# Kernel tuning notes

Measured on AMD Instinct MI355X. Metric: run time of the kernel, lower is better.

The kernel has to match this reference:

```python
import jax, jax.numpy as jnp
from jax import lax
import numpy as np


def _conv4d(x, w, b, stride, padding):
    # Faithful 4D conv emulation: K temporal slices, each its own 3D conv.
    # x: [B,Ci,T,D,H,W]; w: [K,Co,Ci,k,k,k]; b: [K,Co] or None.
    # Quirk preserved: bias b[i] is added once per contributing temporal tap i
    # (the torch code accumulates full conv3d outputs including bias).
    B, Ci, T = x.shape[0], x.shape[1], x.shape[2]
    K = w.shape[0]
    O = (T + 2 * padding - K) // stride + 1
    out = None
    for i in range(K):
        j = np.arange(O) * stride + i - padding          # static input frame idx per output frame
        valid = (j >= 0) & (j < T)
        jc = np.clip(j, 0, T - 1)
        xg = jnp.moveaxis(x[:, :, jc], 2, 1)             # [B,O,Ci,D,H,W]
        xg = xg.reshape(B * O, Ci, x.shape[3], x.shape[4], x.shape[5])
        y = lax.conv_general_dilated(xg, w[i], (stride,) * 3, [(padding, padding)] * 3,
                                     dimension_numbers=('NCDHW', 'OIDHW', 'NCDHW'))
        if b is not None:
            y = y + b[i][None, :, None, None, None]
        y = y.reshape(B, O, y.shape[1], y.shape[2], y.shape[3], y.shape[4])
        y = y * jnp.asarray(valid, y.dtype)[None, :, None, None, None, None]
        out = y if out is None else out + y
    return jnp.moveaxis(out, 1, 2)                       # [B,Co,O,D',H',W']


def _maxpool4d(x, k, s, p):
    # pool3d-per-frame then pool1d over T == one 4D max pool (max commutes)
    return lax.reduce_window(x, jnp.array(-jnp.inf, x.dtype), lax.max,
                             (1, 1, k, k, k, k), (1, 1, s, s, s, s),
                             [(0, 0), (0, 0)] + [(p, p)] * 4)


def _avgpool4d_2(x):
    # avg-of-avgs over a full (2,2,2,2) window == 4D average
    s = lax.reduce_window(x, jnp.array(0.0, x.dtype), lax.add,
                          (1, 1, 2, 2, 2, 2), (1,) * 6, [(0, 0)] * 6)
    return s / jnp.asarray(16.0, x.dtype)


def _block(x, w1, b1, w2, b2, stride, dw):
    y = jax.nn.relu(_conv4d(x, w1, b1, stride, 1))
    y = _conv4d(y, w2, b2, 1, 1)
    res = x if dw is None else _conv4d(x, dw, None, stride, 0)
    return jax.nn.relu(y + res)


def _forward(x, conv1_w, l1_w1, l1_b1, l1_w2, l1_b2,
             l2_w1, l2_b1, l2_w2, l2_b2, l2_dw,
             l3_w1, l3_b1, l3_w2, l3_b2, l3_dw,
             l4_w1, l4_b1, l4_w2, l4_b2, l4_dw, fc_w, fc_b):
    h = x[:, None]                                       # [B,1,T,D,H,W]
    h = jax.nn.relu(_conv4d(h, conv1_w, None, 2, 3))     # 36 -> 18
    h = _maxpool4d(h, 3, 2, 1)                           # 18 -> 9
    h = _block(h, l1_w1, l1_b1, l1_w2, l1_b2, 1, None)   # 9
    h = _block(h, l2_w1, l2_b1, l2_w2, l2_b2, 2, l2_dw)  # 9 -> 5
    h = _block(h, l3_w1, l3_b1, l3_w2, l3_b2, 2, l3_dw)  # 5 -> 3
    h = _block(h, l4_w1, l4_b1, l4_w2, l4_b2, 2, l4_dw)  # 3 -> 2
    h = _avgpool4d_2(h)                                  # 2 -> 1
    h = h.reshape(-1, 512)
    return h @ fc_w.T + fc_b


def setup_inputs() -> dict:
    key = jax.random.key(0)
    ks = jax.random.split(key, 40)
    ctr = iter(range(40))
    def w(shape, fan):
        return jax.random.normal(ks[next(ctr)], shape, jnp.float32) * np.float32(np.sqrt(2.0 / fan))
    def bias(shape):
        return jax.random.normal(ks[next(ctr)], shape, jnp.float32) * np.float32(0.01)
    d = {}
    d['x'] = jax.random.normal(ks[next(ctr)], (1, 36, 36, 36, 36), jnp.float32)
    d['conv1_w'] = w((7, 64, 1, 7, 7, 7), 343)
    d['l1_w1'] = w((3, 64, 64, 3, 3, 3), 64 * 27); d['l1_b1'] = bias((3, 64))
    d['l1_w2'] = w((3, 64, 64, 3, 3, 3), 64 * 27); d['l1_b2'] = bias((3, 64))
    d['l2_w1'] = w((3, 128, 64, 3, 3, 3), 64 * 27); d['l2_b1'] = bias((3, 128))
    d['l2_w2'] = w((3, 128, 128, 3, 3, 3), 128 * 27); d['l2_b2'] = bias((3, 128))
    d['l2_dw'] = w((1, 128, 64, 1, 1, 1), 64)
    d['l3_w1'] = w((3, 256, 128, 3, 3, 3), 128 * 27); d['l3_b1'] = bias((3, 256))
    d['l3_w2'] = w((3, 256, 256, 3, 3, 3), 256 * 27); d['l3_b2'] = bias((3, 256))
    d['l3_dw'] = w((1, 256, 128, 1, 1, 1), 128)
    d['l4_w1'] = w((3, 512, 256, 3, 3, 3), 256 * 27); d['l4_b1'] = bias((3, 512))
    d['l4_w2'] = w((3, 512, 512, 3, 3, 3), 512 * 27); d['l4_b2'] = bias((3, 512))
    d['l4_dw'] = w((1, 512, 256, 1, 1, 1), 256)
    d['fc_w'] = w((1, 512), 512); d['fc_b'] = bias((1,))
    return d


def reference(x, conv1_w, l1_w1, l1_b1, l1_w2, l1_b2,
              l2_w1, l2_b1, l2_w2, l2_b2, l2_dw,
              l3_w1, l3_b1, l3_w2, l3_b2, l3_dw,
              l4_w1, l4_b1, l4_w2, l4_b2, l4_dw, fc_w, fc_b):
    return _forward(x, conv1_w, l1_w1, l1_b1, l1_w2, l1_b2,
                    l2_w1, l2_b1, l2_w2, l2_b2, l2_dw,
                    l3_w1, l3_b1, l3_w2, l3_b2, l3_dw,
                    l4_w1, l4_b1, l4_w2, l4_b2, l4_dw, fc_w, fc_b)
```

## Files before the change

### kernel.cpp

```cpp
#include <hip/hip_runtime.h>

typedef __bf16 bf16x8 __attribute__((ext_vector_type(8)));
typedef float f32x4 __attribute__((ext_vector_type(4)));
typedef unsigned short ushortT;

__device__ __forceinline__ unsigned short f2bf(float f) {
    unsigned u = __float_as_uint(f);
    u += 0x7fffu + ((u >> 16) & 1u);
    return (unsigned short)(u >> 16);
}
__device__ __forceinline__ float bf2f(unsigned short h) {
    return __uint_as_float((unsigned)h << 16);
}

__global__ __launch_bounds__(256) void prep0(const float* __restrict__ x,
                                             const float* __restrict__ c1w,
                                             ushortT* __restrict__ xp,
                                             ushortT* __restrict__ o1) {
    int bid = blockIdx.x, tid = threadIdx.x;
    if (bid < 1737) {
        long idx = (long)bid * 256 + tid;
        if (idx >= 444528L) return;
        int q = (int)(idx % 6); long r = idx / 6;
        int h = (int)(r % 42); r /= 42;
        int d = (int)(r % 42); int t = (int)(r / 42);
        int tt = t - 3, dd = d - 3, hh = h - 3;
        bool rok = ((unsigned)tt < 36u) && ((unsigned)dd < 36u) && ((unsigned)hh < 36u);
        const float* src = x + (((long)tt * 36 + dd) * 36 + hh) * 36;
        union { ushortT s[8]; uint4 u; } v;
#pragma unroll
        for (int j = 0; j < 8; ++j) {
            int ww = q * 8 + j - 3;
            float f = (rok && (unsigned)ww < 36u) ? src[ww] : 0.f;
            v.s[j] = f2bf(f);
        }
        *(uint4*)(xp + idx * 8) = v.u;
    } else {
        int e = (bid - 1737) * 256 + tid;
        if (e < 200704) {
            int k = e % 3136, co = e / 3136;
            int kw = k & 7, kh = (k >> 3) & 7, kdt = k >> 6;
            int kt = kdt / 7, kd = kdt % 7;
            float v = 0.f;
            if (kh < 7 && kw < 7)
                v = c1w[(size_t)(kt * 64 + co) * 343 + kd * 49 + kh * 7 + kw];
            o1[e] = f2bf(v);
        }
    }
}

__global__ __launch_bounds__(128) void mega_kernel(
        const ushortT* __restrict__ xp, const ushortT* __restrict__ aw,
        ushortT* __restrict__ outc1,
        const float* __restrict__ w11, const float* __restrict__ w12,
        const float* __restrict__ w21, const float* __restrict__ w22,
        const float* __restrict__ w31, const float* __restrict__ w32,
        const float* __restrict__ w41, const float* __restrict__ w42,
        ushortT* __restrict__ o11, ushortT* __restrict__ o12,
        ushortT* __restrict__ o21, ushortT* __restrict__ o22,
        ushortT* __restrict__ o31, ushortT* __restrict__ o32,
        ushortT* __restrict__ o41, ushortT* __restrict__ o42) {
    __shared__ __align__(16) ushortT smem[9520];
    int bid = blockIdx.x, tid = threadIdx.x;

    if (bid < 1350) {
        int wt = bid % 5; int r = bid / 5;
        int ht = r % 5; r /= 5;
        int dt = r % 3; int ot = r / 3;
        int ow0 = wt * 4, oh0 = ht * 4, od0 = dt * 6;
        int gw0 = 2 * ow0, gh0 = 2 * oh0, gd0 = 2 * od0;

        int lane = tid & 63, wv = tid >> 6;
        int l15 = lane & 15, g = lane >> 4;
        int dh = l15 >> 2, dw = l15 & 3;

        const ushortT* ap0 = aw + (size_t)(wv * 32 + l15) * 3136 + g * 8;
        const ushortT* ap1 = ap0 + 16 * 3136;

        ushortT* curb = smem;
        ushortT* nxtb = smem + 4760;

        auto stage = [&](ushortT* buf, int kt) {
            int gt = 2 * ot + kt;
            for (int rr = tid; rr < 238; rr += 128) {
                int ld = rr / 14, lh = rr - ld * 14;
                const ushortT* s = xp +
                    ((size_t)((gt * 42 + gd0 + ld) * 42 + gh0 + lh)) * 48 + gw0;
                uint4 a = *(const uint4*)s;
                uint4 b = *(const uint4*)(s + 8);
                ushortT* d = buf + rr * 20;
                *(uint2*)(d)      = make_uint2(a.x, a.y);
                *(uint2*)(d + 4)  = make_uint2(a.z, a.w);
                *(uint2*)(d + 8)  = make_uint2(b.x, b.y);
                *(uint2*)(d + 12) = make_uint2(b.z, b.w);
            }
        };

        f32x4 acc[2][6];
#pragma unroll
        for (int c = 0; c < 2; ++c)
#pragma unroll
            for (int m = 0; m < 6; ++m) acc[c][m] = (f32x4){0.f, 0.f, 0.f, 0.f};

        stage(curb, 0);
        __syncthreads();

        int lhl = (2 * dh + g) * 20 + 2 * dw;
        int kidx = 0;
        for (int kt = 0; kt < 7; ++kt) {
            if (kt < 6) stage(nxtb, kt + 1);
            for (int kd = 0; kd < 7; ++kd) {
                int C0 = kd * 280 + lhl;
#pragma unroll
                for (int khq = 0; khq < 2; ++khq) {
                    bf16x8 a0 = *(const bf16x8*)(ap0 + kidx);
                    bf16x8 a1 = *(const bf16x8*)(ap1 + kidx);
                    kidx += 32;
                    int C = C0 + khq * 80;
#pragma unroll
                    for (int m = 0; m < 6; ++m) {
                        int off = C + m * 560;
                        union { unsigned u[4]; bf16x8 v; } bb;
                        bb.u[0] = *(const unsigned*)(curb + off);
                        bb.u[1] = *(const unsigned*)(curb + off + 2);
                        bb.u[2] = *(const unsigned*)(curb + off + 4);
                        bb.u[3] = *(const unsigned*)(curb + off + 6);
                        acc[0][m] = __builtin_amdgcn_mfma_f32_16x16x32_bf16(a0, bb.v, acc[0][m], 0, 0, 0);
                        acc[1][m] = __builtin_amdgcn_mfma_f32_16x16x32_bf16(a1, bb.v, acc[1][m], 0, 0, 0);
                    }
                }
            }
            __syncthreads();
            ushortT* t2 = curb; curb = nxtb; nxtb = t2;
        }

        int oh = oh0 + dh, ow = ow0 + dw;
        if (oh < 18 && ow < 18) {
#pragma unroll
            for (int m = 0; m < 6; ++m) {
                int od = od0 + m;
                int pos = ((ot * 18 + od) * 18 + oh) * 18 + ow;
#pragma unroll
                for (int c = 0; c < 2; ++c) {
                    ushort4 st;
                    st.x = f2bf(fmaxf(acc[c][m][0], 0.f));
                    st.y = f2bf(fmaxf(acc[c][m][1], 0.f));
                    st.z = f2bf(fmaxf(acc[c][m][2], 0.f));
                    st.w = f2bf(fmaxf(acc[c][m][3], 0.f));
                    *(ushort4*)(outc1 + (size_t)pos * 64 + wv * 32 + c * 16 + g * 4) = st;
                }
            }
        }
        return;
    }

    int wb = bid - 1350;
    const float* in; ushortT* out; int Ci, Co, nc, base;
    if (wb < 1536) {
        if (wb < 384) {
            if (wb < 192) { in = w11; out = o11; Ci = 64; Co = 64; nc = 1; base = 0; }
            else          { in = w12; out = o12; Ci = 64; Co = 64; nc = 1; base = 192; }
        } else if (wb < 768) { in = w21; out = o21; Ci = 64;  Co = 128; nc = 1; base = 384; }
        else                 { in = w22; out = o22; Ci = 128; Co = 128; nc = 2; base = 768; }
    } else if (wb < 6144) {
        if (wb < 3072) { in = w31; out = o31; Ci = 128; Co = 256; nc = 2; base = 1536; }
        else           { in = w32; out = o32; Ci = 256; Co = 256; nc = 4; base = 3072; }
    } else {
        if (wb < 12288) { in = w41; out = o41; Ci = 256; Co = 512; nc = 4; base = 6144; }
        else            { in = w42; out = o42; Ci = 512; Co = 512; nc = 8; base = 12288; }
    }
    int lb = wb - base;
    int c64 = lb % nc;
    int co = (lb / nc) % Co;
    int i = lb / (nc * Co);

    const float* src = in + ((size_t)(i * Co + co) * Ci + 64 * c64) * 27;
    float* tile = (float*)smem;
    for (int e = tid; e < 432; e += 128)
        *(float4*)(tile + 4 * e) = *(const float4*)(src + 4 * e);
    __syncthreads();
    ushortT* dst = out + (size_t)(i * 27) * Co * Ci + (size_t)co * Ci + 64 * c64;
    size_t tapstride = (size_t)Co * Ci;
    for (int e = tid; e < 432; e += 128) {
        int tap = e >> 4, q = e & 15;
        ushort4 v;
        v.x = f2bf(tile[(4 * q + 0) * 27 + tap]);
        v.y = f2bf(tile[(4 * q + 1) * 27 + tap]);
        v.z = f2bf(tile[(4 * q + 2) * 27 + tap]);
        v.w = f2bf(tile[(4 * q + 3) * 27 + tap]);
        *(ushort4*)(dst + (size_t)tap * tapstride + 4 * q) = v;
    }
}

__global__ void maxpool2(const ushortT* __restrict__ in, ushortT* __restrict__ out,
                         ushortT* __restrict__ zb) {
    int idx = blockIdx.x * 256 + threadIdx.x;
    if (idx < 128) zb[idx] = 0;
    if (idx >= 6561 * 16) return;
    int c4 = idx & 15;
    int p = idx >> 4;
    int ow = p % 9; int t = p / 9;
    int oh = t % 9; t /= 9;
    int od = t % 9; int ot = t / 9;
    ushort4 m = {0, 0, 0, 0};
    for (int kt = 0; kt < 3; ++kt) { int it = 2 * ot + kt - 1; if ((unsigned)it >= 18u) continue;
        for (int kd = 0; kd < 3; ++kd) { int id = 2 * od + kd - 1; if ((unsigned)id >= 18u) continue;
            for (int kh = 0; kh < 3; ++kh) { int ih = 2 * oh + kh - 1; if ((unsigned)ih >= 18u) continue;
                int rb = ((it * 18 + id) * 18 + ih) * 18;
                for (int kw = 0; kw < 3; ++kw) { int iw = 2 * ow + kw - 1; if ((unsigned)iw >= 18u) continue;
                    ushort4 v = *(const ushort4*)(in + (size_t)(rb + iw) * 64 + c4 * 4);
                    m.x = v.x > m.x ? v.x : m.x;
                    m.y = v.y > m.y ? v.y : m.y;
                    m.z = v.z > m.z ? v.z : m.z;
                    m.w = v.w > m.w ? v.w : m.w;
                }
            }
        }
    }
    *(ushort4*)(out + (size_t)p * 64 + c4 * 4) = m;
}

template <int KC, int FUSE>
__global__ void convmfma(const ushortT* __restrict__ xb, const ushortT* __restrict__ wt,
                         const float* __restrict__ bias, const ushortT* __restrict__ res,
                         ushortT* __restrict__ outb, float* __restrict__ part,
                         const ushortT* __restrict__ zq,
                         int Ci, int Co, int T, int O, int stride, int chunk,
                         const float* __restrict__ dwW, ushortT* __restrict__ dwOut) {
    if (dwW && blockIdx.y == (unsigned)(Co >> 6)) {
        int O2 = O * O, O3 = O2 * O, O4 = O3 * O;
        int total = Co * O4;
        int sthr = gridDim.x * gridDim.z * 256;
        for (int idx = (blockIdx.z * gridDim.x + blockIdx.x) * 256 + threadIdx.x;
             idx < total; idx += sthr) {
            int co = idx % Co;
            int pos = idx / Co;
            int ow = pos % O, oh = (pos / O) % O, od = (pos / O2) % O, ot = pos / O3;
            int ip = (((2 * ot) * T + 2 * od) * T + 2 * oh) * T + 2 * ow;
            const ushortT* xpp = xb + (size_t)ip * Ci;
            const float* wp = dwW + (size_t)co * Ci;
            float acc = 0.f;
            for (int c8 = 0; c8 < Ci; c8 += 8) {
                uint4 xv = *(const uint4*)(xpp + c8);
                float4 w0 = *(const float4*)(wp + c8);
                float4 w1 = *(const float4*)(wp + c8 + 4);
                acc = fmaf(bf2f((unsigned short)(xv.x & 0xffff)), w0.x, acc);
                acc = fmaf(bf2f((unsigned short)(xv.x >> 16)),    w0.y, acc);
                acc = fmaf(bf2f((unsigned short)(xv.y & 0xffff)), w0.z, acc);
                acc = fmaf(bf2f((unsigned short)(xv.y >> 16)),    w0.w, acc);
                acc = fmaf(bf2f((unsigned short)(xv.z & 0xffff)), w1.x, acc);
                acc = fmaf(bf2f((unsigned short)(xv.z >> 16)),    w1.y, acc);
                acc = fmaf(bf2f((unsigned short)(xv.w & 0xffff)), w1.z, acc);
                acc = fmaf(bf2f((unsigned short)(xv.w >> 16)),    w1.w, acc);
            }
            dwOut[idx] = f2bf(acc);
        }
        return;
    }

    int lane = threadIdx.x & 63;
    int wv = threadIdx.x >> 6;
    int p0 = blockIdx.x * 16;
    int co0 = (blockIdx.y * 4 + wv) * 16;
    int cbase = blockIdx.z * chunk;

    int pn = p0 + (lane & 15);
    int O2 = O * O, O3 = O2 * O, O4 = O3 * O;
    bool pv = pn < O4;
    int pc = pv ? pn : 0;
    int ow = pc % O, oh = (pc / O) % O, od = (pc / O2) % O, ot = pc / O3;
    int g = lane >> 4;
    int kl = cbase + g * 8;

    const ushortT* aRow = wt + (size_t)(co0 + (lane & 15)) * Ci + kl;
    size_t tapStride = (size_t)Co * Ci;
    const ushortT* zp = zq + g * 8;

    f32x4 acc = {0.f, 0.f, 0.f, 0.f};

    int itb = ot * stride - 1, idb = od * stride - 1, ihb = oh * stride - 1, iwb = ow * stride - 1;

    for (int i = 0; i < 3; ++i) {
        int it = itb + i;
        bool vt = pv && ((unsigned)it < (unsigned)T);
        for (int kd = 0; kd < 3; ++kd) {
            int id = idb + kd;
            bool vdd = vt && ((unsigned)id < (unsigned)T);
            int btd = (it * T + id) * T;
            for (int kh = 0; kh < 3; ++kh) {
                int ih = ihb + kh;
                bool vh = vdd && ((unsigned)ih < (unsigned)T);
                for (int kw = 0; kw < 3; ++kw) {
                    int iw = iwb + kw;
                    bool v = vh && ((unsigned)iw < (unsigned)T);
                    int ip = (btd + ih) * T + iw;
                    const ushortT* bp = v ? (xb + (size_t)ip * Ci + kl) : zp;
                    int tapIdx = (i * 9 + kd * 3 + kh) * 3 + kw;
                    const ushortT* apw = aRow + (size_t)tapIdx * tapStride;
#pragma unroll
                    for (int kc = 0; kc < KC; ++kc) {
                        bf16x8 av = *(const bf16x8*)(apw + kc * 32);
                        bf16x8 bv = *(const bf16x8*)(bp + kc * 32);
                        acc = __builtin_amdgcn_mfma_f32_16x16x32_bf16(av, bv, acc, 0, 0, 0);
                    }
                }
            }
        }
    }

    if (!pv) return;
    int cob = co0 + g * 4;
    if (FUSE) {
        float bb[4] = {0.f, 0.f, 0.f, 0.f};
        for (int i = 0; i < 3; ++i) {
            int it = itb + i;
            if ((unsigned)it < (unsigned)T) {
#pragma unroll
                for (int r = 0; r < 4; ++r) bb[r] += bias[i * Co + cob + r];
            }
        }
        float rv[4] = {0.f, 0.f, 0.f, 0.f};
        if (res) {
            ushort4 rr = *(const ushort4*)(res + (size_t)pn * Co + cob);
            rv[0] = bf2f(rr.x); rv[1] = bf2f(rr.y); rv[2] = bf2f(rr.z); rv[3] = bf2f(rr.w);
        }
        ushort4 st;
        st.x = f2bf(fmaxf(acc[0] + bb[0] + rv[0], 0.f));
        st.y = f2bf(fmaxf(acc[1] + bb[1] + rv[1], 0.f));
        st.z = f2bf(fmaxf(acc[2] + bb[2] + rv[2], 0.f));
        st.w = f2bf(fmaxf(acc[3] + bb[3] + rv[3], 0.f));
        *(ushort4*)(outb + (size_t)pn * Co + cob) = st;
    } else {
        *(f32x4*)(part + ((size_t)blockIdx.z * O4 + pn) * Co + cob) = acc;
    }
}

__global__ void finalize_k(const float* __restrict__ part, int KS,
                           const float* __restrict__ bias, const ushortT* __restrict__ res,
                           ushortT* __restrict__ outb, int Co, int O4, int T, int O, int stride,
                           int total) {
    int idx = blockIdx.x * 256 + threadIdx.x;
    if (idx >= total) return;
    int co = idx % Co;
    int pos = idx / Co;
    float v = 0.f;
    for (int z = 0; z < KS; ++z) v += part[((size_t)z * O4 + pos) * Co + co];
    int ot = pos / (O * O * O);
    for (int i = 0; i < 3; ++i) {
        int it = ot * stride + i - 1;
        if ((unsigned)it < (unsigned)T) v += bias[i * Co + co];
    }
    if (res) v += bf2f(res[idx]);
    outb[idx] = f2bf(fmaxf(v, 0.f));
}

__global__ void avgfc2(const ushortT* __restrict__ xin, const float* __restrict__ fw,
                       const float* __restrict__ fb, float* __restrict__ out) {
    __shared__ float ls[8];
    int t = threadIdx.x;
    float s = 0.f;
#pragma unroll
    for (int pp = 0; pp < 16; ++pp) s += bf2f(xin[pp * 512 + t]);
    s = s * (1.f / 16.f) * fw[t];
    for (int off = 32; off > 0; off >>= 1) s += __shfl_xor(s, off, 64);
    if ((t & 63) == 0) ls[t >> 6] = s;
    __syncthreads();
    if (t == 0) {
        float tot = 0.f;
#pragma unroll
        for (int i = 0; i < 8; ++i) tot += ls[i];
        out[0] = tot + fb[0];
    }
}

extern "C" void kernel_launch(void* const* d_in, const int* in_sizes, int n_in,
                              void* d_out, int out_size, void* d_ws, size_t ws_size,
                              hipStream_t stream) {
    const float* x       = (const float*)d_in[0];
    const float* conv1_w = (const float*)d_in[1];
    const float* l1_w1 = (const float*)d_in[2];
    const float* l1_b1 = (const float*)d_in[3];
    const float* l1_w2 = (const float*)d_in[4];
    const float* l1_b2 = (const float*)d_in[5];
    const float* l2_w1 = (const float*)d_in[6];
    const float* l2_b1 = (const float*)d_in[7];
    const float* l2_w2 = (const float*)d_in[8];
    const float* l2_b2 = (const float*)d_in[9];
    const float* l2_dw = (const float*)d_in[10];
    const float* l3_w1 = (const float*)d_in[11];
    const float* l3_b1 = (const float*)d_in[12];
    const float* l3_w2 = (const float*)d_in[13];
    const float* l3_b2 = (const float*)d_in[14];
    const float* l3_dw = (const float*)d_in[15];
    const float* l4_w1 = (const float*)d_in[16];
    const float* l4_b1 = (const float*)d_in[17];
    const float* l4_w2 = (const float*)d_in[18];
    const float* l4_b2 = (const float*)d_in[19];
    const float* l4_dw = (const float*)d_in[20];
    const float* fc_w  = (const float*)d_in[21];
    const float* fc_b  = (const float*)d_in[22];
    float* outp = (float*)d_out;

    char* bp = (char*)d_ws;
    auto alloc = [&](size_t bytes) {
        char* r = bp;
        bp += (bytes + 255) & ~(size_t)255;
        return (void*)r;
    };
    ushortT* A16 = (ushortT*)alloc(6718464ull * 2);
    ushortT* XP  = (ushortT*)alloc(3556224ull * 2);
    ushortT* Aw1 = (ushortT*)alloc(200704ull * 2);
    ushortT* X0 = (ushortT*)alloc(419904ull * 2);
    ushortT* Y1 = (ushortT*)alloc(419904ull * 2);
    ushortT* X1 = (ushortT*)alloc(419904ull * 2);
    ushortT* Y2 = (ushortT*)alloc(80000ull * 2);
    ushortT* R2 = (ushortT*)alloc(80000ull * 2);
    ushortT* X2 = (ushortT*)alloc(80000ull * 2);
    ushortT* Y3 = (ushortT*)alloc(20736ull * 2);
    ushortT* R3 = (ushortT*)alloc(20736ull * 2);
    ushortT* X3 = (ushortT*)alloc(20736ull * 2);
    ushortT* Y4 = (ushortT*)alloc(8192ull * 2);
    ushortT* R4 = (ushortT*)alloc(8192ull * 2);
    ushortT* X4 = (ushortT*)alloc(8192ull * 2);
    ushortT* W11 = (ushortT*)alloc(331776ull * 2);
    ushortT* W12 = (ushortT*)alloc(331776ull * 2);
    ushortT* W21 = (ushortT*)alloc(663552ull * 2);
    ushortT* W22 = (ushortT*)alloc(1327104ull * 2);
    ushortT* W31 = (ushortT*)alloc(2654208ull * 2);
    ushortT* W32 = (ushortT*)alloc(5308416ull * 2);
    ushortT* W41 = (ushortT*)alloc(10616832ull * 2);
    ushortT* W42 = (ushortT*)alloc(21233664ull * 2);
    float* P    = (float*)alloc(165888ull * 4);
    ushortT* ZB = (ushortT*)alloc(256);
    if ((size_t)(bp - (char*)d_ws) > ws_size) return;

    prep0<<<2521, 256, 0, stream>>>(x, conv1_w, XP, Aw1);

    mega_kernel<<<25926, 128, 0, stream>>>(XP, Aw1, A16,
                                           l1_w1, l1_w2, l2_w1, l2_w2, l3_w1, l3_w2,
                                           l4_w1, l4_w2,
                                           W11, W12, W21, W22, W31, W32, W41, W42);

    maxpool2<<<411, 256, 0, stream>>>(A16, X0, ZB);

    convmfma<2, 1><<<dim3(411, 1, 1), 256, 0, stream>>>(X0, W11, l1_b1, nullptr, Y1, nullptr,
                                                        ZB, 64, 64, 9, 9, 1, 64,
                                                        nullptr, nullptr);
    convmfma<2, 1><<<dim3(411, 1, 1), 256, 0, stream>>>(Y1, W12, l1_b2, X0, X1, nullptr,
                                                        ZB, 64, 64, 9, 9, 1, 64,
                                                        nullptr, nullptr);

    convmfma<2, 1><<<dim3(40, 3, 1), 256, 0, stream>>>(X1, W21, l2_b1, nullptr, Y2, nullptr,
                                                       ZB, 64, 128, 9, 5, 2, 64,
                                                       l2_dw, R2);
    convmfma<4, 1><<<dim3(40, 2, 1), 256, 0, stream>>>(Y2, W22, l2_b2, R2, X2, nullptr,
                                                       ZB, 128, 128, 5, 5, 1, 128,
                                                       nullptr, nullptr);

    convmfma<1, 0><<<dim3(6, 5, 4), 256, 0, stream>>>(X2, W31, nullptr, nullptr, nullptr, P,
                                                      ZB, 128, 256, 5, 3, 2, 32,
                                                      l3_dw, R3);
    finalize_k<<<81, 256, 0, stream>>>(P, 4, l3_b1, nullptr, Y3, 256, 81, 5, 3, 2, 20736);
    convmfma<1, 0><<<dim3(6, 4, 8), 256, 0, stream>>>(Y3, W32, nullptr, nullptr, nullptr, P,
                                                      ZB, 256, 256, 3, 3, 1, 32,
                                                      nullptr, nullptr);
    finalize_k<<<81, 256, 0, stream>>>(P, 8, l3_b2, R3, X3, 256, 81, 3, 3, 1, 20736);

    convmfma<1, 0><<<dim3(1, 9, 8), 256, 0, stream>>>(X3, W41, nullptr, nullptr, nullptr, P,
                                                      ZB, 256, 512, 3, 2, 2, 32,
                                                      l4_dw, R4);
    finalize_k<<<32, 256, 0, stream>>>(P, 8, l4_b1, nullptr, Y4, 512, 16, 3, 2, 2, 8192);
    convmfma<1, 0><<<dim3(1, 8, 16), 256, 0, stream>>>(Y4, W42, nullptr, nullptr, nullptr, P,
                                                       ZB, 512, 512, 2, 2, 1, 32,
                                                       nullptr, nullptr);
    finalize_k<<<32, 256, 0, stream>>>(P, 16, l4_b2, R4, X4, 512, 16, 2, 2, 1, 8192);

    avgfc2<<<1, 512, 0, stream>>>(X4, fc_w, fc_b, outp);
}
```

Baseline: 547.2 us.

## Fuse trunk layers into one persistent kernel with grid barriers; pad conv1 smem rows

Replaces the chain of maxpool, per-layer convmfma, finalize and avgfc launches with a single persistent kernel of 512 blocks. Stages are separated by a software grid barrier built on atomics, which removes per-launch overhead and gaps between the many small late layers. Also pads the conv1 shared-memory row stride from 20 to 22 elements to reduce LDS bank conflicts. The cost is that convolution units lose their compile-time KC unrolling, and the grid barrier relies on all 512 blocks being co-resident, otherwise it can deadlock.

New measurement: 1.164 ms. 113% more time.

```diff
diff --git a/kernel.cpp b/kernel.cpp
--- a/kernel.cpp
+++ b/kernel.cpp
@@ -3,6 +3,8 @@
 typedef __bf16 bf16x8 __attribute__((ext_vector_type(8)));
 typedef float f32x4 __attribute__((ext_vector_type(4)));
 typedef unsigned short ushortT;
+
+#define NB 512
 
 __device__ __forceinline__ unsigned short f2bf(float f) {
     unsigned u = __float_as_uint(f);
@@ -16,8 +18,14 @@
 __global__ __launch_bounds__(256) void prep0(const float* __restrict__ x,
                                              const float* __restrict__ c1w,
                                              ushortT* __restrict__ xp,
-                                             ushortT* __restrict__ o1) {
+                                             ushortT* __restrict__ o1,
+                                             ushortT* __restrict__ zb,
+                                             int* __restrict__ bar) {
     int bid = blockIdx.x, tid = threadIdx.x;
+    if (bid == 0) {
+        if (tid < 128) zb[tid] = 0;
+        if (tid == 128) { bar[0] = 0; bar[1] = 0; }
+    }
     if (bid < 1737) {
         long idx = (long)bid * 256 + tid;
         if (idx >= 444528L) return;
@@ -60,7 +68,7 @@
         ushortT* __restrict__ o21, ushortT* __restrict__ o22,
         ushortT* __restrict__ o31, ushortT* __restrict__ o32,
         ushortT* __restrict__ o41, ushortT* __restrict__ o42) {
-    __shared__ __align__(16) ushortT smem[9520];
+    __shared__ __align__(16) ushortT smem[10472];
     int bid = blockIdx.x, tid = threadIdx.x;
 
     if (bid < 1350) {
@@ -78,7 +86,7 @@
         const ushortT* ap1 = ap0 + 16 * 3136;
 
         ushortT* curb = smem;
-        ushortT* nxtb = smem + 4760;
+        ushortT* nxtb = smem + 5236;
 
         auto stage = [&](ushortT* buf, int kt) {
             int gt = 2 * ot + kt;
@@ -88,11 +96,9 @@
                     ((size_t)((gt * 42 + gd0 + ld) * 42 + gh0 + lh)) * 48 + gw0;
                 uint4 a = *(const uint4*)s;
                 uint4 b = *(const uint4*)(s + 8);
-                ushortT* d = buf + rr * 20;
-                *(uint2*)(d)      = make_uint2(a.x, a.y);
-                *(uint2*)(d + 4)  = make_uint2(a.z, a.w);
-                *(uint2*)(d + 8)  = make_uint2(b.x, b.y);
-                *(uint2*)(d + 12) = make_uint2(b.z, b.w);
+                unsigned* d = (unsigned*)buf + rr * 11;
+                d[0] = a.x; d[1] = a.y; d[2] = a.z; d[3] = a.w;
+                d[4] = b.x; d[5] = b.y; d[6] = b.z; d[7] = b.w;
             }
         };
 
@@ -105,21 +111,21 @@
         stage(curb, 0);
         __syncthreads();
 
-        int lhl = (2 * dh + g) * 20 + 2 * dw;
+        int lhl = (2 * dh + g) * 22 + 2 * dw;
         int kidx = 0;
         for (int kt = 0; kt < 7; ++kt) {
             if (kt < 6) stage(nxtb, kt + 1);
             for (int kd = 0; kd < 7; ++kd) {
-                int C0 = kd * 280 + lhl;
+                int C0 = kd * 308 + lhl;
 #pragma unroll
                 for (int khq = 0; khq < 2; ++khq) {
                     bf16x8 a0 = *(const bf16x8*)(ap0 + kidx);
                     bf16x8 a1 = *(const bf16x8*)(ap1 + kidx);
                     kidx += 32;
-                    int C = C0 + khq * 80;
+                    int C = C0 + khq * 88;
 #pragma unroll
                     for (int m = 0; m < 6; ++m) {
-                        int off = C + m * 560;
+                        int off = C + m * 616;
                         union { unsigned u[4]; bf16x8 v; } bb;
                         bb.u[0] = *(const unsigned*)(curb + off);
                         bb.u[1] = *(const unsigned*)(curb + off + 2);
@@ -192,77 +198,35 @@
     }
 }
 
-__global__ void maxpool2(const ushortT* __restrict__ in, ushortT* __restrict__ out,
-                         ushortT* __restrict__ zb) {
-    int idx = blockIdx.x * 256 + threadIdx.x;
-    if (idx < 128) zb[idx] = 0;
-    if (idx >= 6561 * 16) return;
-    int c4 = idx & 15;
-    int p = idx >> 4;
-    int ow = p % 9; int t = p / 9;
-    int oh = t % 9; t /= 9;
-    int od = t % 9; int ot = t / 9;
-    ushort4 m = {0, 0, 0, 0};
-    for (int kt = 0; kt < 3; ++kt) { int it = 2 * ot + kt - 1; if ((unsigned)it >= 18u) continue;
-        for (int kd = 0; kd < 3; ++kd) { int id = 2 * od + kd - 1; if ((unsigned)id >= 18u) continue;
-            for (int kh = 0; kh < 3; ++kh) { int ih = 2 * oh + kh - 1; if ((unsigned)ih >= 18u) continue;
-                int rb = ((it * 18 + id) * 18 + ih) * 18;
-                for (int kw = 0; kw < 3; ++kw) { int iw = 2 * ow + kw - 1; if ((unsigned)iw >= 18u) continue;
-                    ushort4 v = *(const ushort4*)(in + (size_t)(rb + iw) * 64 + c4 * 4);
-                    m.x = v.x > m.x ? v.x : m.x;
-                    m.y = v.y > m.y ? v.y : m.y;
-                    m.z = v.z > m.z ? v.z : m.z;
-                    m.w = v.w > m.w ? v.w : m.w;
-                }
-            }
-        }
-    }
-    *(ushort4*)(out + (size_t)p * 64 + c4 * 4) = m;
-}
-
-template <int KC, int FUSE>
-__global__ void convmfma(const ushortT* __restrict__ xb, const ushortT* __restrict__ wt,
-                         const float* __restrict__ bias, const ushortT* __restrict__ res,
-                         ushortT* __restrict__ outb, float* __restrict__ part,
-                         const ushortT* __restrict__ zq,
-                         int Ci, int Co, int T, int O, int stride, int chunk,
-                         const float* __restrict__ dwW, ushortT* __restrict__ dwOut) {
-    if (dwW && blockIdx.y == (unsigned)(Co >> 6)) {
-        int O2 = O * O, O3 = O2 * O, O4 = O3 * O;
-        int total = Co * O4;
-        int sthr = gridDim.x * gridDim.z * 256;
-        for (int idx = (blockIdx.z * gridDim.x + blockIdx.x) * 256 + threadIdx.x;
-             idx < total; idx += sthr) {
-            int co = idx % Co;
-            int pos = idx / Co;
-            int ow = pos % O, oh = (pos / O) % O, od = (pos / O2) % O, ot = pos / O3;
-            int ip = (((2 * ot) * T + 2 * od) * T + 2 * oh) * T + 2 * ow;
-            const ushortT* xpp = xb + (size_t)ip * Ci;
-            const float* wp = dwW + (size_t)co * Ci;
-            float acc = 0.f;
-            for (int c8 = 0; c8 < Ci; c8 += 8) {
-                uint4 xv = *(const uint4*)(xpp + c8);
-                float4 w0 = *(const float4*)(wp + c8);
-                float4 w1 = *(const float4*)(wp + c8 + 4);
-                acc = fmaf(bf2f((unsigned short)(xv.x & 0xffff)), w0.x, acc);
-                acc = fmaf(bf2f((unsigned short)(xv.x >> 16)),    w0.y, acc);
-                acc = fmaf(bf2f((unsigned short)(xv.y & 0xffff)), w0.z, acc);
-                acc = fmaf(bf2f((unsigned short)(xv.y >> 16)),    w0.w, acc);
-                acc = fmaf(bf2f((unsigned short)(xv.z & 0xffff)), w1.x, acc);
-                acc = fmaf(bf2f((unsigned short)(xv.z >> 16)),    w1.y, acc);
-                acc = fmaf(bf2f((unsigned short)(xv.w & 0xffff)), w1.z, acc);
-                acc = fmaf(bf2f((unsigned short)(xv.w >> 16)),    w1.w, acc);
-            }
-            dwOut[idx] = f2bf(acc);
-        }
-        return;
-    }
-
+
+__device__ __forceinline__ void gbar(int* cnt, int* gen) {
+    __syncthreads();
+    if (threadIdx.x == 0) {
+        __threadfence();
+        int g = atomicAdd(gen, 0);
+        if (atomicAdd(cnt, 1) == NB - 1) {
+            atomicExch(cnt, 0);
+            __threadfence();
+            atomicAdd(gen, 1);
+        } else {
+            while (atomicAdd(gen, 0) == g) __builtin_amdgcn_s_sleep(2);
+        }
+        __threadfence();
+    }
+    __syncthreads();
+}
+
+__device__ __noinline__ void conv_unit(const ushortT* xb, const ushortT* wt,
+                                       const float* bias, const ushortT* res,
+                                       ushortT* outb, float* part, const ushortT* zq,
+                                       int Ci, int Co, int T, int O, int stride, int chunk,
+                                       int pblk, int cog, int ks, bool fuse) {
     int lane = threadIdx.x & 63;
     int wv = threadIdx.x >> 6;
-    int p0 = blockIdx.x * 16;
-    int co0 = (blockIdx.y * 4 + wv) * 16;
-    int cbase = blockIdx.z * chunk;
+    int p0 = pblk * 16;
+    int co0 = (cog * 4 + wv) * 16;
+    int cbase = ks * chunk;
+    int nkc = chunk >> 5;
 
     int pn = p0 + (lane & 15);
     int O2 = O * O, O3 = O2 * O, O4 = O3 * O;
@@ -297,8 +261,7 @@
                     const ushortT* bp = v ? (xb + (size_t)ip * Ci + kl) : zp;
                     int tapIdx = (i * 9 + kd * 3 + kh) * 3 + kw;
                     const ushortT* apw = aRow + (size_t)tapIdx * tapStride;
-#pragma unroll
-                    for (int kc = 0; kc < KC; ++kc) {
+                    for (int kc = 0; kc < nkc; ++kc) {
                         bf16x8 av = *(const bf16x8*)(apw + kc * 32);
                         bf16x8 bv = *(const bf16x8*)(bp + kc * 32);
                         acc = __builtin_amdgcn_mfma_f32_16x16x32_bf16(av, bv, acc, 0, 0, 0);
@@ -310,19 +273,19 @@
 
     if (!pv) return;
     int cob = co0 + g * 4;
-    if (FUSE) {
+    if (fuse) {
         float bb[4] = {0.f, 0.f, 0.f, 0.f};
         for (int i = 0; i < 3; ++i) {
             int it = itb + i;
             if ((unsigned)it < (unsigned)T) {
 #pragma unroll
-                for (int r = 0; r < 4; ++r) bb[r] += bias[i * Co + cob + r];
+                for (int rr = 0; rr < 4; ++rr) bb[rr] += bias[i * Co + cob + rr];
             }
         }
         float rv[4] = {0.f, 0.f, 0.f, 0.f};
         if (res) {
-            ushort4 rr = *(const ushort4*)(res + (size_t)pn * Co + cob);
-            rv[0] = bf2f(rr.x); rv[1] = bf2f(rr.y); rv[2] = bf2f(rr.z); rv[3] = bf2f(rr.w);
+            ushort4 r4 = *(const ushort4*)(res + (size_t)pn * Co + cob);
+            rv[0] = bf2f(r4.x); rv[1] = bf2f(r4.y); rv[2] = bf2f(r4.z); rv[3] = bf2f(r4.w);
         }
         ushort4 st;
         st.x = f2bf(fmaxf(acc[0] + bb[0] + rv[0], 0.f));
@@ -331,45 +294,169 @@
         st.w = f2bf(fmaxf(acc[3] + bb[3] + rv[3], 0.f));
         *(ushort4*)(outb + (size_t)pn * Co + cob) = st;
     } else {
-        *(f32x4*)(part + ((size_t)blockIdx.z * O4 + pn) * Co + cob) = acc;
-    }
-}
-
-__global__ void finalize_k(const float* __restrict__ part, int KS,
-                           const float* __restrict__ bias, const ushortT* __restrict__ res,
-                           ushortT* __restrict__ outb, int Co, int O4, int T, int O, int stride,
-                           int total) {
-    int idx = blockIdx.x * 256 + threadIdx.x;
-    if (idx >= total) return;
-    int co = idx % Co;
-    int pos = idx / Co;
-    float v = 0.f;
-    for (int z = 0; z < KS; ++z) v += part[((size_t)z * O4 + pos) * Co + co];
-    int ot = pos / (O * O * O);
-    for (int i = 0; i < 3; ++i) {
-        int it = ot * stride + i - 1;
-        if ((unsigned)it < (unsigned)T) v += bias[i * Co + co];
-    }
-    if (res) v += bf2f(res[idx]);
-    outb[idx] = f2bf(fmaxf(v, 0.f));
-}
-
-__global__ void avgfc2(const ushortT* __restrict__ xin, const float* __restrict__ fw,
-                       const float* __restrict__ fb, float* __restrict__ out) {
-    __shared__ float ls[8];
-    int t = threadIdx.x;
-    float s = 0.f;
-#pragma unroll
-    for (int pp = 0; pp < 16; ++pp) s += bf2f(xin[pp * 512 + t]);
-    s = s * (1.f / 16.f) * fw[t];
-    for (int off = 32; off > 0; off >>= 1) s += __shfl_xor(s, off, 64);
-    if ((t & 63) == 0) ls[t >> 6] = s;
-    __syncthreads();
-    if (t == 0) {
-        float tot = 0.f;
-#pragma unroll
-        for (int i = 0; i < 8; ++i) tot += ls[i];
-        out[0] = tot + fb[0];
+        *(f32x4*)(part + ((size_t)ks * O4 + pn) * Co + cob) = acc;
+    }
+}
+
+__device__ __noinline__ void dw_all(const ushortT* xb, const float* w, ushortT* out,
+                                    int Ci, int Co, int T, int O, int total) {
+    int O2 = O * O, O3 = O2 * O;
+    for (int idx = blockIdx.x * 256 + threadIdx.x; idx < total; idx += NB * 256) {
+        int co = idx % Co;
+        int pos = idx / Co;
+        int ow = pos % O, oh = (pos / O) % O, od = (pos / O2) % O, ot = pos / O3;
+        int ip = (((2 * ot) * T + 2 * od) * T + 2 * oh) * T + 2 * ow;
+        const ushortT* xp = xb + (size_t)ip * Ci;
+        const float* wp = w + (size_t)co * Ci;
+        float acc = 0.f;
+        for (int c8 = 0; c8 < Ci; c8 += 8) {
+            uint4 xv = *(const uint4*)(xp + c8);
+            float4 w0 = *(const float4*)(wp + c8);
+            float4 w1 = *(const float4*)(wp + c8 + 4);
+            acc = fmaf(bf2f((unsigned short)(xv.x & 0xffff)), w0.x, acc);
+            acc = fmaf(bf2f((unsigned short)(xv.x >> 16)),    w0.y, acc);
+            acc = fmaf(bf2f((unsigned short)(xv.y & 0xffff)), w0.z, acc);
+            acc = fmaf(bf2f((unsigned short)(xv.y >> 16)),    w0.w, acc);
+            acc = fmaf(bf2f((unsigned short)(xv.z & 0xffff)), w1.x, acc);
+            acc = fmaf(bf2f((unsigned short)(xv.z >> 16)),    w1.y, acc);
+            acc = fmaf(bf2f((unsigned short)(xv.w & 0xffff)), w1.z, acc);
+            acc = fmaf(bf2f((unsigned short)(xv.w >> 16)),    w1.w, acc);
+        }
+        out[idx] = f2bf(acc);
+    }
+}
+
+__device__ __noinline__ void fin_all(const float* part, int KS, const float* bias,
+                                     const ushortT* res, ushortT* outb,
+                                     int Co, int O4, int T, int O, int stride, int total) {
+    for (int idx = blockIdx.x * 256 + threadIdx.x; idx < total; idx += NB * 256) {
+        int co = idx % Co;
+        int pos = idx / Co;
+        float v = 0.f;
+        for (int z = 0; z < KS; ++z) v += part[((size_t)z * O4 + pos) * Co + co];
+        int ot = pos / (O * O * O);
+        for (int i = 0; i < 3; ++i) {
+            int it = ot * stride + i - 1;
+            if ((unsigned)it < (unsigned)T) v += bias[i * Co + co];
+        }
+        if (res) v += bf2f(res[idx]);
+        outb[idx] = f2bf(fmaxf(v, 0.f));
+    }
+}
+
+__global__ __launch_bounds__(256, 2) void trunk(
+        const ushortT* __restrict__ A16,
+        ushortT* __restrict__ X0, ushortT* __restrict__ Y1, ushortT* __restrict__ X1,
+        ushortT* __restrict__ Y2, ushortT* __restrict__ R2, ushortT* __restrict__ X2,
+        ushortT* __restrict__ Y3, ushortT* __restrict__ R3, ushortT* __restrict__ X3,
+        ushortT* __restrict__ Y4, ushortT* __restrict__ R4, ushortT* __restrict__ X4,
+        const ushortT* __restrict__ W11, const ushortT* __restrict__ W12,
+        const ushortT* __restrict__ W21, const ushortT* __restrict__ W22,
+        const ushortT* __restrict__ W31, const ushortT* __restrict__ W32,
+        const ushortT* __restrict__ W41, const ushortT* __restrict__ W42,
+        const float* __restrict__ b11, const float* __restrict__ b12,
+        const float* __restrict__ b21, const float* __restrict__ b22,
+        const float* __restrict__ b31, const float* __restrict__ b32,
+        const float* __restrict__ b41, const float* __restrict__ b42,
+        const float* __restrict__ dw2, const float* __restrict__ dw3,
+        const float* __restrict__ dw4,
+        const float* __restrict__ fcw, const float* __restrict__ fcb,
+        float* __restrict__ outp,
+        float* __restrict__ P, const ushortT* __restrict__ ZB, int* __restrict__ bar) {
+    __shared__ float ls[4];
+    int bid = blockIdx.x, tid = threadIdx.x;
+    int* cnt = bar; int* gen = bar + 1;
+
+    for (int idx = bid * 256 + tid; idx < 6561 * 16; idx += NB * 256) {
+        int c4 = idx & 15;
+        int p = idx >> 4;
+        int ow = p % 9; int t = p / 9;
+        int oh = t % 9; t /= 9;
+        int od = t % 9; int ot = t / 9;
+        ushort4 m = {0, 0, 0, 0};
+        for (int kt = 0; kt < 3; ++kt) { int it = 2 * ot + kt - 1; if ((unsigned)it >= 18u) continue;
+            for (int kd = 0; kd < 3; ++kd) { int id = 2 * od + kd - 1; if ((unsigned)id >= 18u) continue;
+                for (int kh = 0; kh < 3; ++kh) { int ih = 2 * oh + kh - 1; if ((unsigned)ih >= 18u) continue;
+                    int rb = ((it * 18 + id) * 18 + ih) * 18;
+                    for (int kw = 0; kw < 3; ++kw) { int iw = 2 * ow + kw - 1; if ((unsigned)iw >= 18u) continue;
+                        ushort4 v = *(const ushort4*)(A16 + (size_t)(rb + iw) * 64 + c4 * 4);
+                        m.x = v.x > m.x ? v.x : m.x;
+                        m.y = v.y > m.y ? v.y : m.y;
+                        m.z = v.z > m.z ? v.z : m.z;
+                        m.w = v.w > m.w ? v.w : m.w;
+                    }
+                }
+            }
+        }
+        *(ushort4*)(X0 + (size_t)p * 64 + c4 * 4) = m;
+    }
+    gbar(cnt, gen);
+
+    for (int u = bid; u < 411; u += NB)
+        conv_unit(X0, W11, b11, nullptr, Y1, nullptr, ZB, 64, 64, 9, 9, 1, 64, u, 0, 0, true);
+    gbar(cnt, gen);
+
+    for (int u = bid; u < 411; u += NB)
+        conv_unit(Y1, W12, b12, X0, X1, nullptr, ZB, 64, 64, 9, 9, 1, 64, u, 0, 0, true);
+    gbar(cnt, gen);
+
+    for (int u = bid; u < 80; u += NB)
+        conv_unit(X1, W21, b21, nullptr, Y2, nullptr, ZB, 64, 128, 9, 5, 2, 64,
+                  u % 40, u / 40, 0, true);
+    dw_all(X1, dw2, R2, 64, 128, 9, 5, 80000);
+    gbar(cnt, gen);
+
+    for (int u = bid; u < 80; u += NB)
+        conv_unit(Y2, W22, b22, R2, X2, nullptr, ZB, 128, 128, 5, 5, 1, 128,
+                  u % 40, u / 40, 0, true);
+    gbar(cnt, gen);
+
+    for (int u = bid; u < 96; u += NB)
+        conv_unit(X2, W31, nullptr, nullptr, nullptr, P, ZB, 128, 256, 5, 3, 2, 32,
+                  u % 6, (u / 6) % 4, u / 24, false);
+    dw_all(X2, dw3, R3, 128, 256, 5, 3, 20736);
+    gbar(cnt, gen);
+
+    fin_all(P, 4, b31, nullptr, Y3, 256, 81, 5, 3, 2, 20736);
+    gbar(cnt, gen);
+
+    for (int u = bid; u < 192; u += NB)
+        conv_unit(Y3, W32, nullptr, nullptr, nullptr, P, ZB, 256, 256, 3, 3, 1, 32,
+                  u % 6, (u / 6) % 4, u / 24, false);
+    gbar(cnt, gen);
+
+    fin_all(P, 8, b32, R3, X3, 256, 81, 3, 3, 1, 20736);
+    gbar(cnt, gen);
+
+    for (int u = bid; u < 64; u += NB)
+        conv_unit(X3, W41, nullptr, nullptr, nullptr, P, ZB, 256, 512, 3, 2, 2, 32,
+                  0, u % 8, u / 8, false);
+    dw_all(X3, dw4, R4, 256, 512, 3, 2, 8192);
+    gbar(cnt, gen);
+
+    fin_all(P, 8, b41, nullptr, Y4, 512, 16, 3, 2, 2, 8192);
+    gbar(cnt, gen);
+
+    for (int u = bid; u < 128; u += NB)
+        conv_unit(Y4, W42, nullptr, nullptr, nullptr, P, ZB, 512, 512, 2, 2, 1, 32,
+                  0, u % 8, u / 8, false);
+    gbar(cnt, gen);
+
+    fin_all(P, 16, b42, R4, X4, 512, 16, 2, 2, 1, 8192);
+    gbar(cnt, gen);
+
+    if (bid == 0) {
+        float s = 0.f;
+        for (int c = tid; c < 512; c += 256) {
+            float a = 0.f;
+#pragma unroll
+            for (int pp = 0; pp < 16; ++pp) a += bf2f(X4[pp * 512 + c]);
+            s += a * (1.f / 16.f) * fcw[c];
+        }
+        for (int off = 32; off > 0; off >>= 1) s += __shfl_xor(s, off, 64);
+        if ((tid & 63) == 0) ls[tid >> 6] = s;
+        __syncthreads();
+        if (tid == 0) outp[0] = ls[0] + ls[1] + ls[2] + ls[3] + fcb[0];
     }
 }
 
@@ -432,48 +519,21 @@
     ushortT* W42 = (ushortT*)alloc(21233664ull * 2);
     float* P    = (float*)alloc(165888ull * 4);
     ushortT* ZB = (ushortT*)alloc(256);
+    int* BAR    = (int*)alloc(256);
     if ((size_t)(bp - (char*)d_ws) > ws_size) return;
 
-    prep0<<<2521, 256, 0, stream>>>(x, conv1_w, XP, Aw1);
+    prep0<<<2521, 256, 0, stream>>>(x, conv1_w, XP, Aw1, ZB, BAR);
 
     mega_kernel<<<25926, 128, 0, stream>>>(XP, Aw1, A16,
                                            l1_w1, l1_w2, l2_w1, l2_w2, l3_w1, l3_w2,
                                            l4_w1, l4_w2,
                                            W11, W12, W21, W22, W31, W32, W41, W42);
 
-    maxpool2<<<411, 256, 0, stream>>>(A16, X0, ZB);
-
-    convmfma<2, 1><<<dim3(411, 1, 1), 256, 0, stream>>>(X0, W11, l1_b1, nullptr, Y1, nullptr,
-                                                        ZB, 64, 64, 9, 9, 1, 64,
-                                                        nullptr, nullptr);
-    convmfma<2, 1><<<dim3(411, 1, 1), 256, 0, stream>>>(Y1, W12, l1_b2, X0, X1, nullptr,
-                                                        ZB, 64, 64, 9, 9, 1, 64,
-                                                        nullptr, nullptr);
-
-    convmfma<2, 1><<<dim3(40, 3, 1), 256, 0, stream>>>(X1, W21, l2_b1, nullptr, Y2, nullptr,
-                                                       ZB, 64, 128, 9, 5, 2, 64,
-                                                       l2_dw, R2);
-    convmfma<4, 1><<<dim3(40, 2, 1), 256, 0, stream>>>(Y2, W22, l2_b2, R2, X2, nullptr,
-                                                       ZB, 128, 128, 5, 5, 1, 128,
-                                                       nullptr, nullptr);
-
-    convmfma<1, 0><<<dim3(6, 5, 4), 256, 0, stream>>>(X2, W31, nullptr, nullptr, nullptr, P,
-                                                      ZB, 128, 256, 5, 3, 2, 32,
-                                                      l3_dw, R3);
-    finalize_k<<<81, 256, 0, stream>>>(P, 4, l3_b1, nullptr, Y3, 256, 81, 5, 3, 2, 20736);
-    convmfma<1, 0><<<dim3(6, 4, 8), 256, 0, stream>>>(Y3, W32, nullptr, nullptr, nullptr, P,
-                                                      ZB, 256, 256, 3, 3, 1, 32,
-                                                      nullptr, nullptr);
-    finalize_k<<<81, 256, 0, stream>>>(P, 8, l3_b2, R3, X3, 256, 81, 3, 3, 1, 20736);
-
-    convmfma<1, 0><<<dim3(1, 9, 8), 256, 0, stream>>>(X3, W41, nullptr, nullptr, nullptr, P,
-                                                      ZB, 256, 512, 3, 2, 2, 32,
-                                                      l4_dw, R4);
-    finalize_k<<<32, 256, 0, stream>>>(P, 8, l4_b1, nullptr, Y4, 512, 16, 3, 2, 2, 8192);
-    convmfma<1, 0><<<dim3(1, 8, 16), 256, 0, stream>>>(Y4, W42, nullptr, nullptr, nullptr, P,
-                                                       ZB, 512, 512, 2, 2, 1, 32,
-                                                       nullptr, nullptr);
-    finalize_k<<<32, 256, 0, stream>>>(P, 16, l4_b2, R4, X4, 512, 16, 2, 2, 1, 8192);
-
-    avgfc2<<<1, 512, 0, stream>>>(X4, fc_w, fc_b, outp);
-}
+    trunk<<<NB, 256, 0, stream>>>(A16,
+                                  X0, Y1, X1, Y2, R2, X2, Y3, R3, X3, Y4, R4, X4,
+                                  W11, W12, W21, W22, W31, W32, W41, W42,
+                                  l1_b1, l1_b2, l2_b1, l2_b2, l3_b1, l3_b2, l4_b1, l4_b2,
+                                  l2_dw, l3_dw, l4_dw,
+                                  fc_w, fc_b, outp,
+                                  P, ZB, BAR);
+}
```
